# Performance work log

Measured on AMD Instinct MI355X. Metric: run time of the kernel, lower is better.

## Reference

```python
import jax, jax.numpy as jnp
import numpy as np

B, T, N, H, D = 8, 128, 170, 4, 16
F = H * D  # 64
LN_EPS = 1e-5
MASK_FILL = -(2.0 ** 15) + 1.0  # -32767, matches torch code


def setup_inputs() -> dict:
    key = jax.random.key(0)
    ks = jax.random.split(key, 16)
    s = 0.05
    def w(k):
        return jax.random.normal(k, (F, F), jnp.float32) * s
    def b(k):
        return jax.random.normal(k, (F,), jnp.float32) * s
    return {
        "x": jax.random.normal(ks[0], (B, T, N, F), jnp.float32),
        "te": jax.random.normal(ks[1], (B, T, N, F), jnp.float32),
        "Wq": w(ks[2]), "bq": b(ks[3]),
        "Wk": w(ks[4]), "bk": b(ks[5]),
        "Wv": w(ks[6]), "bv": b(ks[7]),
        "Wo": w(ks[8]), "bo": b(ks[9]),
        "Wf1": w(ks[10]), "bf1": b(ks[11]),
        "Wf2": w(ks[12]), "bf2": b(ks[13]),
    }


def _ln(v):
    # LayerNorm over last dim, elementwise_affine=False
    m = jnp.mean(v, axis=-1, keepdims=True)
    var = jnp.mean((v - m) ** 2, axis=-1, keepdims=True)
    return (v - m) / jnp.sqrt(var + LN_EPS)


def reference(x, te, Wq, bq, Wk, bk, Wv, bv, Wo, bo, Wf1, bf1, Wf2, bf2):
    x = x + te  # [B,T,N,F]
    # q/k/v projections (FeedForward with L=1 -> plain linear, no ReLU)
    q = (x @ Wq + bq).reshape(B, T, N, H, D)
    k = (x @ Wk + bk).reshape(B, T, N, H, D)
    v = (x @ Wv + bv).reshape(B, T, N, H, D)
    # attention over time axis, independent per node n and head h
    att = jnp.einsum('btnhd,bsnhd->bhnts', q, k) / jnp.sqrt(jnp.float32(D))
    causal = jnp.tril(jnp.ones((T, T), dtype=bool))  # keep s <= t
    att = jnp.where(causal[None, None, None, :, :], att, MASK_FILL)
    att = jax.nn.softmax(att, axis=-1)
    out = jnp.einsum('bhnts,bsnhd->btnhd', att, v).reshape(B, T, N, F)
    out = out @ Wo + bo  # ofc
    val = _ln(out + x)
    # ff: Linear-ReLU-Linear with residual + LN (res_ln=True)
    ff = jax.nn.relu(val @ Wf1 + bf1) @ Wf2 + bf2
    return _ln(ff + val)
```

## Files before the change

### kernel.cpp

```cpp
#include <hip/hip_runtime.h>

typedef __attribute__((ext_vector_type(8))) short short8;
typedef __attribute__((ext_vector_type(4))) float f32x4;
typedef __attribute__((ext_vector_type(16))) float f32x16;

#define B_ 8
#define T_ 128
#define N_ 170
#define F_ 64
#define ROWSTRIDE (N_ * F_)

union U4 { unsigned u[4]; short8 s; };

__device__ __forceinline__ unsigned short f2bf(float f) {
    union { float f; unsigned u; } v; v.f = f;
    unsigned r = v.u + 0x7fffu + ((v.u >> 16) & 1u);
    return (unsigned short)(r >> 16);
}
__device__ __forceinline__ unsigned cvtpk(float lo, float hi) {
    unsigned d;
    asm("v_cvt_pk_bf16_f32 %0, %1, %2" : "=v"(d) : "v"(lo), "v"(hi));
    return d;
}
__device__ __forceinline__ int swz128(int row, int byteInRow) {
    return row * 128 + (byteInRow ^ ((row & 7) << 4));
}
__device__ __forceinline__ int swz256(int row, int byteInRow) {
    return row * 256 + (byteInRow ^ ((row & 15) << 4));
}
__device__ __forceinline__ short8 ldfrag16(const char* base, int row0, int kbyte, int lane) {
    int row = row0 + (lane & 15);
    return *(const short8*)(base + swz128(row, kbyte + ((lane >> 4) << 4)));
}
__device__ __forceinline__ short8 ldfrag16w(const char* base, int row0, int kbyte, int lane) {
    int row = row0 + (lane & 15);
    return *(const short8*)(base + swz256(row, kbyte + ((lane >> 4) << 4)));
}
__device__ __forceinline__ short8 ldfrag32(const char* base, int row0, int colbyte, int lane) {
    int row = row0 + (lane & 31);
    return *(const short8*)(base + swz128(row, colbyte + ((lane >> 5) << 4)));
}
__device__ __forceinline__ short8 wfragT(const unsigned short* __restrict__ wT, int nt, int kc, int lane) {
    int j  = nt * 16 + (lane & 15);
    int k0 = kc * 32 + ((lane >> 4) & 3) * 8;
    return *(const short8*)(wT + j * 64 + k0);
}
__device__ __forceinline__ f32x4 zero4() {
    f32x4 v = {0.f, 0.f, 0.f, 0.f};
    return v;
}
__device__ __forceinline__ f32x16 zero16() {
    f32x16 v = {0.f, 0.f, 0.f, 0.f, 0.f, 0.f, 0.f, 0.f,
                0.f, 0.f, 0.f, 0.f, 0.f, 0.f, 0.f, 0.f};
    return v;
}
__device__ __forceinline__ float rmax16(const f32x16& v) {
    float a0 = fmaxf(v[0], v[1]),  a1 = fmaxf(v[2], v[3]);
    float a2 = fmaxf(v[4], v[5]),  a3 = fmaxf(v[6], v[7]);
    float a4 = fmaxf(v[8], v[9]),  a5 = fmaxf(v[10], v[11]);
    float a6 = fmaxf(v[12], v[13]), a7 = fmaxf(v[14], v[15]);
    float b0 = fmaxf(a0, a1), b1 = fmaxf(a2, a3);
    float b2 = fmaxf(a4, a5), b3 = fmaxf(a6, a7);
    return fmaxf(fmaxf(b0, b1), fmaxf(b2, b3));
}
__device__ __forceinline__ float rsum16(const f32x16& v) {
    float a0 = v[0] + v[1],  a1 = v[2] + v[3];
    float a2 = v[4] + v[5],  a3 = v[6] + v[7];
    float a4 = v[8] + v[9],  a5 = v[10] + v[11];
    float a6 = v[12] + v[13], a7 = v[14] + v[15];
    float b0 = a0 + a1, b1 = a2 + a3, b2 = a4 + a5, b3 = a6 + a7;
    return (b0 + b1) + (b2 + b3);
}

__device__ __forceinline__ void lnS(float (&z)[2][4][4]) {
#pragma unroll
    for (int mi = 0; mi < 2; ++mi) {
        float s = 0.f;
#pragma unroll
        for (int nt = 0; nt < 4; ++nt)
#pragma unroll
        for (int r = 0; r < 4; ++r) s += z[mi][nt][r];
        s += __shfl_xor(s, 16); s += __shfl_xor(s, 32);
        float mean = s * 0.015625f;
        float q = 0.f;
#pragma unroll
        for (int nt = 0; nt < 4; ++nt)
#pragma unroll
        for (int r = 0; r < 4; ++r) { z[mi][nt][r] -= mean; q += z[mi][nt][r] * z[mi][nt][r]; }
        q += __shfl_xor(q, 16); q += __shfl_xor(q, 32);
        float rstd = __builtin_amdgcn_rsqf(q * 0.015625f + 1e-5f);
#pragma unroll
        for (int nt = 0; nt < 4; ++nt)
#pragma unroll
        for (int r = 0; r < 4; ++r) z[mi][nt][r] *= rstd;
    }
}

__global__ void prep_weights(const float* __restrict__ Wq, const float* __restrict__ Wk,
                             const float* __restrict__ Wv, const float* __restrict__ Wo,
                             const float* __restrict__ Wf1, const float* __restrict__ Wf2,
                             unsigned short* __restrict__ ws) {
    const float* Ws[6] = {Wq, Wk, Wv, Wo, Wf1, Wf2};
    const float* W = Ws[blockIdx.x];
    unsigned short* o = ws + blockIdx.x * 4096;
#pragma unroll
    for (int i = 0; i < 16; ++i) {
        int idx = i * 256 + threadIdx.x;
        int j = idx >> 6, k = idx & 63;
        o[idx] = f2bf(W[k * 64 + j]);
    }
}

__global__ __launch_bounds__(256, 4)
void ta_fused(const float* __restrict__ x, const float* __restrict__ te,
              const unsigned short* __restrict__ wT,
              const float* __restrict__ bq, const float* __restrict__ bk,
              const float* __restrict__ bv, const float* __restrict__ bo,
              const float* __restrict__ bf1, const float* __restrict__ bf2,
              float* __restrict__ out)
{
    __shared__ __align__(16) char sKb[16384];
    __shared__ __align__(16) char sVt[16384];

    const int tid  = threadIdx.x;
    const int lane = tid & 63;
    const int wv   = tid >> 6;
    const int lam  = lane & 15;
    const int g    = (lane >> 4) & 3;
    const int bid  = blockIdx.x;
    const int b    = bid / N_;
    const int n    = bid - b * N_;
    const long long base = ((long long)b * T_ * N_ + n) * F_;
    const int t0w = wv * 32;

    short8 ax[2][2];
#pragma unroll
    for (int mi = 0; mi < 2; ++mi) {
        const float* xr = x  + base + (long long)(t0w + mi * 16 + lam) * ROWSTRIDE;
        const float* tr = te + base + (long long)(t0w + mi * 16 + lam) * ROWSTRIDE;
#pragma unroll
        for (int kc = 0; kc < 2; ++kc) {
            int f0 = kc * 32 + g * 8;
            float4 a0 = *(const float4*)(xr + f0);
            float4 a1 = *(const float4*)(xr + f0 + 4);
            float4 c0 = *(const float4*)(tr + f0);
            float4 c1 = *(const float4*)(tr + f0 + 4);
            U4 u;
            u.u[0] = cvtpk(a0.x + c0.x, a0.y + c0.y);
            u.u[1] = cvtpk(a0.z + c0.z, a0.w + c0.w);
            u.u[2] = cvtpk(a1.x + c1.x, a1.y + c1.y);
            u.u[3] = cvtpk(a1.z + c1.z, a1.w + c1.w);
            ax[mi][kc] = u.s;
        }
    }

    short8 qf[4];

    {
        {
            const unsigned short* wTp = wT;
            short8 bw[4][2]; float4 bj[4];
#pragma unroll
            for (int nt = 0; nt < 4; ++nt) {
                bw[nt][0] = wfragT(wTp, nt, 0, lane);
                bw[nt][1] = wfragT(wTp, nt, 1, lane);
                bj[nt]    = *(const float4*)(bq + nt * 16 + g * 4);
            }
            f32x4 acc[2][4];
#pragma unroll
            for (int mi = 0; mi < 2; ++mi)
#pragma unroll
            for (int nt = 0; nt < 4; ++nt) acc[mi][nt] = zero4();
#pragma unroll
            for (int kc = 0; kc < 2; ++kc)
#pragma unroll
            for (int mi = 0; mi < 2; ++mi)
#pragma unroll
            for (int nt = 0; nt < 4; ++nt)
                acc[mi][nt] = __builtin_amdgcn_mfma_f32_16x16x32_bf16(bw[nt][kc], ax[mi][kc], acc[mi][nt], 0, 0, 0);
#pragma unroll
            for (int mi = 0; mi < 2; ++mi)
#pragma unroll
            for (int nt = 0; nt < 4; ++nt) {
                unsigned d0 = cvtpk(acc[mi][nt][0] + bj[nt].x, acc[mi][nt][1] + bj[nt].y);
                unsigned d1 = cvtpk(acc[mi][nt][2] + bj[nt].z, acc[mi][nt][3] + bj[nt].w);
                unsigned long long pk = (unsigned long long)d0 | ((unsigned long long)d1 << 32);
                *(unsigned long long*)(sKb + swz128(t0w + mi * 16 + lam, (nt * 16 + g * 4) * 2)) = pk;
            }
#pragma unroll
            for (int h = 0; h < 4; ++h) qf[h] = ldfrag32(sKb, t0w, h * 32, lane);
        }
        {
            const unsigned short* wTp = wT + 4096;
            short8 bw[4][2]; float4 bj[4];
#pragma unroll
            for (int nt = 0; nt < 4; ++nt) {
                bw[nt][0] = wfragT(wTp, nt, 0, lane);
                bw[nt][1] = wfragT(wTp, nt, 1, lane);
                bj[nt]    = *(const float4*)(bk + nt * 16 + g * 4);
            }
            f32x4 acc[2][4];
#pragma unroll
            for (int mi = 0; mi < 2; ++mi)
#pragma unroll
            for (int nt = 0; nt < 4; ++nt) acc[mi][nt] = zero4();
#pragma unroll
            for (int kc = 0; kc < 2; ++kc)
#pragma unroll
            for (int mi = 0; mi < 2; ++mi)
#pragma unroll
            for (int nt = 0; nt < 4; ++nt)
                acc[mi][nt] = __builtin_amdgcn_mfma_f32_16x16x32_bf16(bw[nt][kc], ax[mi][kc], acc[mi][nt], 0, 0, 0);
#pragma unroll
            for (int mi = 0; mi < 2; ++mi)
#pragma unroll
            for (int nt = 0; nt < 4; ++nt) {
                unsigned d0 = cvtpk(acc[mi][nt][0] + bj[nt].x, acc[mi][nt][1] + bj[nt].y);
                unsigned d1 = cvtpk(acc[mi][nt][2] + bj[nt].z, acc[mi][nt][3] + bj[nt].w);
                unsigned long long pk = (unsigned long long)d0 | ((unsigned long long)d1 << 32);
                *(unsigned long long*)(sKb + swz128(t0w + mi * 16 + lam, (nt * 16 + g * 4) * 2)) = pk;
            }
        }
        {
            const unsigned short* wTp = wT + 2 * 4096;
            short8 bw[4][2]; float bias[4];
#pragma unroll
            for (int nt = 0; nt < 4; ++nt) {
                bw[nt][0] = wfragT(wTp, nt, 0, lane);
                bw[nt][1] = wfragT(wTp, nt, 1, lane);
                bias[nt]  = bv[nt * 16 + lam];
            }
            f32x4 acc[2][4];
#pragma unroll
            for (int mi = 0; mi < 2; ++mi)
#pragma unroll
            for (int nt = 0; nt < 4; ++nt) acc[mi][nt] = zero4();
#pragma unroll
            for (int kc = 0; kc < 2; ++kc)
#pragma unroll
            for (int mi = 0; mi < 2; ++mi)
#pragma unroll
            for (int nt = 0; nt < 4; ++nt)
                acc[mi][nt] = __builtin_amdgcn_mfma_f32_16x16x32_bf16(ax[mi][kc], bw[nt][kc], acc[mi][nt], 0, 0, 0);
#pragma unroll
            for (int mi = 0; mi < 2; ++mi)
#pragma unroll
            for (int nt = 0; nt < 4; ++nt) {
                int f   = nt * 16 + lam;
                int tb0 = t0w + mi * 16 + g * 4;
                unsigned d0 = cvtpk(acc[mi][nt][0] + bias[nt], acc[mi][nt][1] + bias[nt]);
                unsigned d1 = cvtpk(acc[mi][nt][2] + bias[nt], acc[mi][nt][3] + bias[nt]);
                unsigned long long pkv = (unsigned long long)d0 | ((unsigned long long)d1 << 32);
                *(unsigned long long*)(sVt + swz256(f, tb0 * 2)) = pkv;
            }
        }
    }
    __syncthreads();

    f32x4 oaccT[4][2];
    {
        const int tcol = lane & 31;
        const int hi4  = (lane >> 5) * 4;
#pragma unroll
        for (int h = 0; h < 4; ++h) { oaccT[h][0] = zero4(); oaccT[h][1] = zero4(); }

#pragma unroll
        for (int h = 0; h < 4; ++h) {
            f32x16 sacc[4];
            __builtin_amdgcn_s_setprio(1);
#pragma unroll
            for (int sb = 0; sb < 4; ++sb) {
                if (sb > wv) continue;
                short8 kf = ldfrag32(sKb, sb * 32, h * 32, lane);
                sacc[sb] = __builtin_amdgcn_mfma_f32_32x32x16_bf16(kf, qf[h], zero16(), 0, 0, 0);
            }
            __builtin_amdgcn_s_setprio(0);
#pragma unroll
            for (int sb = 0; sb < 4; ++sb) {
                if (sb != wv) continue;
#pragma unroll
                for (int r = 0; r < 16; ++r) {
                    int srow = (r & 3) + 8 * (r >> 2) + hi4;
                    if (srow > tcol) sacc[sb][r] = -3.0e38f;
                }
            }
            float m = -3.0e38f;
#pragma unroll
            for (int sb = 0; sb < 4; ++sb) {
                if (sb > wv) continue;
                m = fmaxf(m, rmax16(sacc[sb]));
            }
            m = fmaxf(m, __shfl_xor(m, 32));
            float sum = 0.f;
#pragma unroll
            for (int sb = 0; sb < 4; ++sb) {
                if (sb > wv) continue;
#pragma unroll
                for (int r = 0; r < 16; ++r)
                    sacc[sb][r] = __expf((sacc[sb][r] - m) * 0.25f);
                sum += rsum16(sacc[sb]);
            }
            sum += __shfl_xor(sum, 32);
            float rs = __builtin_amdgcn_rcpf(sum);

#pragma unroll
            for (int sb = 0; sb < 4; ++sb) {
                if (sb > wv) continue;
                float ps[16];
#pragma unroll
                for (int r = 0; r < 16; ++r) ps[r] = sacc[sb][r] * rs;
                unsigned a0 = cvtpk(ps[0],  ps[1]);
                unsigned a1 = cvtpk(ps[4],  ps[5]);
                unsigned a2 = cvtpk(ps[8],  ps[9]);
                unsigned a3 = cvtpk(ps[12], ps[13]);
                unsigned b0 = cvtpk(ps[2],  ps[3]);
                unsigned b1 = cvtpk(ps[6],  ps[7]);
                unsigned b2 = cvtpk(ps[10], ps[11]);
                unsigned b3 = cvtpk(ps[14], ps[15]);
                asm("v_permlane32_swap_b32 %0, %1" : "+v"(a0), "+v"(a2));
                asm("v_permlane32_swap_b32 %0, %1" : "+v"(a1), "+v"(a3));
                asm("v_permlane16_swap_b32 %0, %1" : "+v"(a0), "+v"(a1));
                asm("v_permlane16_swap_b32 %0, %1" : "+v"(a2), "+v"(a3));
                asm("v_permlane32_swap_b32 %0, %1" : "+v"(b0), "+v"(b2));
                asm("v_permlane32_swap_b32 %0, %1" : "+v"(b1), "+v"(b3));
                asm("v_permlane16_swap_b32 %0, %1" : "+v"(b0), "+v"(b1));
                asm("v_permlane16_swap_b32 %0, %1" : "+v"(b2), "+v"(b3));
                U4 F0, F1;
                F0.u[0] = a0; F0.u[1] = b0; F0.u[2] = a2; F0.u[3] = b2;
                F1.u[0] = a1; F1.u[1] = b1; F1.u[2] = a3; F1.u[3] = b3;
                short8 vf = ldfrag16w(sVt, h * 16, sb * 64, lane);
                __builtin_amdgcn_s_setprio(1);
                oaccT[h][0] = __builtin_amdgcn_mfma_f32_16x16x32_bf16(vf, F0.s, oaccT[h][0], 0, 0, 0);
                oaccT[h][1] = __builtin_amdgcn_mfma_f32_16x16x32_bf16(vf, F1.s, oaccT[h][1], 0, 0, 0);
                __builtin_amdgcn_s_setprio(0);
            }
        }
    }
    __syncthreads();

#pragma unroll
    for (int h = 0; h < 4; ++h)
#pragma unroll
    for (int mi = 0; mi < 2; ++mi) {
        unsigned d0 = cvtpk(oaccT[h][mi][0], oaccT[h][mi][1]);
        unsigned d1 = cvtpk(oaccT[h][mi][2], oaccT[h][mi][3]);
        unsigned long long pk = (unsigned long long)d0 | ((unsigned long long)d1 << 32);
        *(unsigned long long*)(sKb + swz128(t0w + mi * 16 + lam, (h * 16 + g * 4) * 2)) = pk;
    }

    float val[2][4][4];
    {
        short8 af[2][2];
#pragma unroll
        for (int mi = 0; mi < 2; ++mi)
#pragma unroll
        for (int kc = 0; kc < 2; ++kc) af[mi][kc] = ldfrag16(sKb, t0w + mi * 16, kc * 64, lane);
        const unsigned short* wTp = wT + 3 * 4096;
        short8 bwf[4][2]; float4 bj[4];
#pragma unroll
        for (int nt = 0; nt < 4; ++nt) {
            bwf[nt][0] = wfragT(wTp, nt, 0, lane);
            bwf[nt][1] = wfragT(wTp, nt, 1, lane);
            bj[nt]     = *(const float4*)(bo + nt * 16 + g * 4);
        }
        f32x4 acc[2][4];
#pragma unroll
        for (int mi = 0; mi < 2; ++mi)
#pragma unroll
        for (int nt = 0; nt < 4; ++nt) acc[mi][nt] = zero4();
#pragma unroll
        for (int kc = 0; kc < 2; ++kc)
#pragma unroll
        for (int mi = 0; mi < 2; ++mi)
#pragma unroll
        for (int nt = 0; nt < 4; ++nt)
            acc[mi][nt] = __builtin_amdgcn_mfma_f32_16x16x32_bf16(bwf[nt][kc], af[mi][kc], acc[mi][nt], 0, 0, 0);
#pragma unroll
        for (int mi = 0; mi < 2; ++mi)
#pragma unroll
        for (int nt = 0; nt < 4; ++nt) {
            long long roff = base + (long long)(t0w + mi * 16 + lam) * ROWSTRIDE + nt * 16 + g * 4;
            float4 xv = *(const float4*)(x + roff);
            float4 tv = *(const float4*)(te + roff);
            val[mi][nt][0] = acc[mi][nt][0] + bj[nt].x + xv.x + tv.x;
            val[mi][nt][1] = acc[mi][nt][1] + bj[nt].y + xv.y + tv.y;
            val[mi][nt][2] = acc[mi][nt][2] + bj[nt].z + xv.z + tv.z;
            val[mi][nt][3] = acc[mi][nt][3] + bj[nt].w + xv.w + tv.w;
        }
        lnS(val);
#pragma unroll
        for (int mi = 0; mi < 2; ++mi)
#pragma unroll
        for (int nt = 0; nt < 4; ++nt) {
            unsigned d0 = cvtpk(val[mi][nt][0], val[mi][nt][1]);
            unsigned d1 = cvtpk(val[mi][nt][2], val[mi][nt][3]);
            unsigned long long pk = (unsigned long long)d0 | ((unsigned long long)d1 << 32);
            *(unsigned long long*)(sKb + swz128(t0w + mi * 16 + lam, (nt * 16 + g * 4) * 2)) = pk;
        }
    }

    {
        short8 af[2][2];
#pragma unroll
        for (int mi = 0; mi < 2; ++mi)
#pragma unroll
        for (int kc = 0; kc < 2; ++kc) af[mi][kc] = ldfrag16(sKb, t0w + mi * 16, kc * 64, lane);
        const unsigned short* wTp = wT + 4 * 4096;
        short8 bwf[4][2]; float4 bj[4];
#pragma unroll
        for (int nt = 0; nt < 4; ++nt) {
            bwf[nt][0] = wfragT(wTp, nt, 0, lane);
            bwf[nt][1] = wfragT(wTp, nt, 1, lane);
            bj[nt]     = *(const float4*)(bf1 + nt * 16 + g * 4);
        }
        f32x4 acc[2][4];
#pragma unroll
        for (int mi = 0; mi < 2; ++mi)
#pragma unroll
        for (int nt = 0; nt < 4; ++nt) acc[mi][nt] = zero4();
#pragma unroll
        for (int kc = 0; kc < 2; ++kc)
#pragma unroll
        for (int mi = 0; mi < 2; ++mi)
#pragma unroll
        for (int nt = 0; nt < 4; ++nt)
            acc[mi][nt] = __builtin_amdgcn_mfma_f32_16x16x32_bf16(bwf[nt][kc], af[mi][kc], acc[mi][nt], 0, 0, 0);
#pragma unroll
        for (int mi = 0; mi < 2; ++mi)
#pragma unroll
        for (int nt = 0; nt < 4; ++nt) {
            unsigned d0 = cvtpk(fmaxf(acc[mi][nt][0] + bj[nt].x, 0.f), fmaxf(acc[mi][nt][1] + bj[nt].y, 0.f));
            unsigned d1 = cvtpk(fmaxf(acc[mi][nt][2] + bj[nt].z, 0.f), fmaxf(acc[mi][nt][3] + bj[nt].w, 0.f));
            unsigned long long pk = (unsigned long long)d0 | ((unsigned long long)d1 << 32);
            *(unsigned long long*)(sKb + swz128(t0w + mi * 16 + lam, (nt * 16 + g * 4) * 2)) = pk;
        }
    }

    {
        short8 af[2][2];
#pragma unroll
        for (int mi = 0; mi < 2; ++mi)
#pragma unroll
        for (int kc = 0; kc < 2; ++kc) af[mi][kc] = ldfrag16(sKb, t0w + mi * 16, kc * 64, lane);
        const unsigned short* wTp = wT + 5 * 4096;
        short8 bwf[4][2]; float4 bj[4];
#pragma unroll
        for (int nt = 0; nt < 4; ++nt) {
            bwf[nt][0] = wfragT(wTp, nt, 0, lane);
            bwf[nt][1] = wfragT(wTp, nt, 1, lane);
            bj[nt]     = *(const float4*)(bf2 + nt * 16 + g * 4);
        }
        f32x4 acc[2][4];
#pragma unroll
        for (int mi = 0; mi < 2; ++mi)
#pragma unroll
        for (int nt = 0; nt < 4; ++nt) acc[mi][nt] = zero4();
#pragma unroll
        for (int kc = 0; kc < 2; ++kc)
#pragma unroll
        for (int mi = 0; mi < 2; ++mi)
#pragma unroll
        for (int nt = 0; nt < 4; ++nt)
            acc[mi][nt] = __builtin_amdgcn_mfma_f32_16x16x32_bf16(bwf[nt][kc], af[mi][kc], acc[mi][nt], 0, 0, 0);
        float z[2][4][4];
#pragma unroll
        for (int mi = 0; mi < 2; ++mi)
#pragma unroll
        for (int nt = 0; nt < 4; ++nt) {
            z[mi][nt][0] = acc[mi][nt][0] + bj[nt].x + val[mi][nt][0];
            z[mi][nt][1] = acc[mi][nt][1] + bj[nt].y + val[mi][nt][1];
            z[mi][nt][2] = acc[mi][nt][2] + bj[nt].z + val[mi][nt][2];
            z[mi][nt][3] = acc[mi][nt][3] + bj[nt].w + val[mi][nt][3];
        }
        lnS(z);
#pragma unroll
        for (int mi = 0; mi < 2; ++mi)
#pragma unroll
        for (int nt = 0; nt < 4; ++nt) {
            float4 o = {z[mi][nt][0], z[mi][nt][1], z[mi][nt][2], z[mi][nt][3]};
            *(float4*)(out + base + (long long)(t0w + mi * 16 + lam) * ROWSTRIDE + nt * 16 + g * 4) = o;
        }
    }
}

extern "C" void kernel_launch(void* const* d_in, const int* in_sizes, int n_in,
                              void* d_out, int out_size, void* d_ws, size_t ws_size,
                              hipStream_t stream) {
    const float* x   = (const float*)d_in[0];
    const float* te  = (const float*)d_in[1];
    const float* Wq  = (const float*)d_in[2];
    const float* bq  = (const float*)d_in[3];
    const float* Wk  = (const float*)d_in[4];
    const float* bk  = (const float*)d_in[5];
    const float* Wv  = (const float*)d_in[6];
    const float* bv  = (const float*)d_in[7];
    const float* Wo  = (const float*)d_in[8];
    const float* bo  = (const float*)d_in[9];
    const float* Wf1 = (const float*)d_in[10];
    const float* bf1 = (const float*)d_in[11];
    const float* Wf2 = (const float*)d_in[12];
    const float* bf2 = (const float*)d_in[13];
    unsigned short* wsT = (unsigned short*)d_ws;

    prep_weights<<<dim3(6), dim3(256), 0, stream>>>(Wq, Wk, Wv, Wo, Wf1, Wf2, wsT);
    ta_fused<<<dim3(B_ * N_), dim3(256), 0, stream>>>(
        x, te, wsT, bq, bk, bv, bo, bf1, bf2, (float*)d_out);
}
```

Baseline: 88.32 us.

## Stream causal softmax without max subtraction and defer normalization to after PV

Drops the running-max pass from the attention softmax. Each score block is exponentiated right after its QK MFMA, summed and fed straight into the PV MFMA, and the accumulated output is scaled by the reciprocal row sum at the end, with the sum shuffled to the matching lanes. This removes the four-block score buffer and the extra passes over it, which lowers register pressure. The launch attribute also changes to target 5 waves per EU. Without max subtraction the exp can overflow if scores get large, so correctness depends on the score range staying moderate.

```diff
diff --git a/kernel.cpp b/kernel.cpp
--- a/kernel.cpp
+++ b/kernel.cpp
@@ -53,23 +53,6 @@
     f32x16 v = {0.f, 0.f, 0.f, 0.f, 0.f, 0.f, 0.f, 0.f,
                 0.f, 0.f, 0.f, 0.f, 0.f, 0.f, 0.f, 0.f};
     return v;
-}
-__device__ __forceinline__ float rmax16(const f32x16& v) {
-    float a0 = fmaxf(v[0], v[1]),  a1 = fmaxf(v[2], v[3]);
-    float a2 = fmaxf(v[4], v[5]),  a3 = fmaxf(v[6], v[7]);
-    float a4 = fmaxf(v[8], v[9]),  a5 = fmaxf(v[10], v[11]);
-    float a6 = fmaxf(v[12], v[13]), a7 = fmaxf(v[14], v[15]);
-    float b0 = fmaxf(a0, a1), b1 = fmaxf(a2, a3);
-    float b2 = fmaxf(a4, a5), b3 = fmaxf(a6, a7);
-    return fmaxf(fmaxf(b0, b1), fmaxf(b2, b3));
-}
-__device__ __forceinline__ float rsum16(const f32x16& v) {
-    float a0 = v[0] + v[1],  a1 = v[2] + v[3];
-    float a2 = v[4] + v[5],  a3 = v[6] + v[7];
-    float a4 = v[8] + v[9],  a5 = v[10] + v[11];
-    float a6 = v[12] + v[13], a7 = v[14] + v[15];
-    float b0 = a0 + a1, b1 = a2 + a3, b2 = a4 + a5, b3 = a6 + a7;
-    return (b0 + b1) + (b2 + b3);
 }
 
 __device__ __forceinline__ void lnS(float (&z)[2][4][4]) {
@@ -111,7 +94,8 @@
     }
 }
 
-__global__ __launch_bounds__(256, 4)
+__global__ __launch_bounds__(256)
+__attribute__((amdgpu_waves_per_eu(5, 5)))
 void ta_fused(const float* __restrict__ x, const float* __restrict__ te,
               const unsigned short* __restrict__ wT,
               const float* __restrict__ bq, const float* __restrict__ bk,
@@ -262,53 +246,33 @@
         const int tcol = lane & 31;
         const int hi4  = (lane >> 5) * 4;
 #pragma unroll
-        for (int h = 0; h < 4; ++h) { oaccT[h][0] = zero4(); oaccT[h][1] = zero4(); }
-
-#pragma unroll
         for (int h = 0; h < 4; ++h) {
-            f32x16 sacc[4];
-            __builtin_amdgcn_s_setprio(1);
+            float sum = 0.f;
+            f32x4 o0 = zero4(), o1 = zero4();
 #pragma unroll
             for (int sb = 0; sb < 4; ++sb) {
                 if (sb > wv) continue;
                 short8 kf = ldfrag32(sKb, sb * 32, h * 32, lane);
-                sacc[sb] = __builtin_amdgcn_mfma_f32_32x32x16_bf16(kf, qf[h], zero16(), 0, 0, 0);
-            }
-            __builtin_amdgcn_s_setprio(0);
-#pragma unroll
-            for (int sb = 0; sb < 4; ++sb) {
-                if (sb != wv) continue;
-#pragma unroll
-                for (int r = 0; r < 16; ++r) {
-                    int srow = (r & 3) + 8 * (r >> 2) + hi4;
-                    if (srow > tcol) sacc[sb][r] = -3.0e38f;
+                __builtin_amdgcn_s_setprio(1);
+                f32x16 s = __builtin_amdgcn_mfma_f32_32x32x16_bf16(kf, qf[h], zero16(), 0, 0, 0);
+                __builtin_amdgcn_s_setprio(0);
+                if (sb == wv) {
+#pragma unroll
+                    for (int r = 0; r < 16; ++r) {
+                        int srow = (r & 3) + 8 * (r >> 2) + hi4;
+                        if (srow > tcol) s[r] = -3.0e38f;
+                    }
                 }
-            }
-            float m = -3.0e38f;
-#pragma unroll
-            for (int sb = 0; sb < 4; ++sb) {
-                if (sb > wv) continue;
-                m = fmaxf(m, rmax16(sacc[sb]));
-            }
-            m = fmaxf(m, __shfl_xor(m, 32));
-            float sum = 0.f;
-#pragma unroll
-            for (int sb = 0; sb < 4; ++sb) {
-                if (sb > wv) continue;
-#pragma unroll
-                for (int r = 0; r < 16; ++r)
-                    sacc[sb][r] = __expf((sacc[sb][r] - m) * 0.25f);
-                sum += rsum16(sacc[sb]);
-            }
-            sum += __shfl_xor(sum, 32);
-            float rs = __builtin_amdgcn_rcpf(sum);
-
-#pragma unroll
-            for (int sb = 0; sb < 4; ++sb) {
-                if (sb > wv) continue;
                 float ps[16];
 #pragma unroll
-                for (int r = 0; r < 16; ++r) ps[r] = sacc[sb][r] * rs;
+                for (int r = 0; r < 16; ++r) ps[r] = __expf(s[r] * 0.25f);
+                {
+                    float a0 = ps[0] + ps[1],  a1 = ps[2] + ps[3];
+                    float a2 = ps[4] + ps[5],  a3 = ps[6] + ps[7];
+                    float a4 = ps[8] + ps[9],  a5 = ps[10] + ps[11];
+                    float a6 = ps[12] + ps[13], a7 = ps[14] + ps[15];
+                    sum += ((a0 + a1) + (a2 + a3)) + ((a4 + a5) + (a6 + a7));
+                }
                 unsigned a0 = cvtpk(ps[0],  ps[1]);
                 unsigned a1 = cvtpk(ps[4],  ps[5]);
                 unsigned a2 = cvtpk(ps[8],  ps[9]);
@@ -330,9 +294,18 @@
                 F1.u[0] = a1; F1.u[1] = b1; F1.u[2] = a3; F1.u[3] = b3;
                 short8 vf = ldfrag16w(sVt, h * 16, sb * 64, lane);
                 __builtin_amdgcn_s_setprio(1);
-                oaccT[h][0] = __builtin_amdgcn_mfma_f32_16x16x32_bf16(vf, F0.s, oaccT[h][0], 0, 0, 0);
-                oaccT[h][1] = __builtin_amdgcn_mfma_f32_16x16x32_bf16(vf, F1.s, oaccT[h][1], 0, 0, 0);
+                o0 = __builtin_amdgcn_mfma_f32_16x16x32_bf16(vf, F0.s, o0, 0, 0, 0);
+                o1 = __builtin_amdgcn_mfma_f32_16x16x32_bf16(vf, F1.s, o1, 0, 0, 0);
                 __builtin_amdgcn_s_setprio(0);
+            }
+            sum += __shfl_xor(sum, 32);
+            float rs = __builtin_amdgcn_rcpf(sum);
+            float rs0 = __shfl(rs, lam);
+            float rs1 = __shfl(rs, lam + 16);
+#pragma unroll
+            for (int r = 0; r < 4; ++r) {
+                oaccT[h][0][r] = o0[r] * rs0;
+                oaccT[h][1][r] = o1[r] * rs1;
             }
         }
     }
```

Result: slower. 107.5 us (+21.7%).
